# Performance work log

Hardware: AMD Instinct MI355X
Metric: run time of the kernel (lower is better)

## Reference

```python
import jax, jax.numpy as jnp
import numpy as np

C = 128
B = 64
EPS = 1e-6


def _ln2d(x, w, b):
    # LayerNorm over channel dim (NAFNet-style LayerNorm2d), eps=1e-6
    mu = x.mean(axis=1, keepdims=True)
    var = ((x - mu) ** 2).mean(axis=1, keepdims=True)
    return (x - mu) / jnp.sqrt(var + EPS) * w[None, :, None, None] + b[None, :, None, None]


def _conv4(x, w, b):
    # Conv2d kernel 4, stride 4, no padding; NCHW / OIHW
    y = jax.lax.conv_general_dilated(x, w, (4, 4), 'VALID',
                                     dimension_numbers=('NCHW', 'OIHW', 'NCHW'))
    return y + b[None, :, None, None]


def _pixel_shuffle4(x):
    # (B, c*16, H, W) -> (B, c, 4H, 4W), torch PixelShuffle semantics
    b, c16, h, w = x.shape
    c = c16 // 16
    x = x.reshape(b, c, 4, 4, h, w)
    x = x.transpose(0, 1, 4, 2, 5, 3)
    return x.reshape(b, c, h * 4, w * 4)


def setup_inputs() -> dict:
    key = jax.random.key(0)
    ks = jax.random.split(key, 16)
    s = 0.02
    return {
        'x_l': jax.random.normal(ks[0], (B, C, 32, 32), jnp.float32),
        'x_r': jax.random.normal(ks[1], (B, C, 32, 32), jnp.float32),
        'ln_w_l': jnp.ones((C,), jnp.float32), 'ln_b_l': jnp.zeros((C,), jnp.float32),
        'ln_w_r': jnp.ones((C,), jnp.float32), 'ln_b_r': jnp.zeros((C,), jnp.float32),
        'Wl1': jax.random.normal(ks[2], (C, C, 4, 4), jnp.float32) * s,
        'bl1': jnp.zeros((C,), jnp.float32),
        'Wr1': jax.random.normal(ks[3], (C, C, 4, 4), jnp.float32) * s,
        'br1': jnp.zeros((C,), jnp.float32),
        'Wl2': jax.random.normal(ks[4], (C, C, 4, 4), jnp.float32) * s,
        'bl2': jnp.zeros((C,), jnp.float32),
        'Wr2': jax.random.normal(ks[5], (C, C, 4, 4), jnp.float32) * s,
        'br2': jnp.zeros((C,), jnp.float32),
        'pos': jax.random.normal(ks[6], (1, C, 8, 8), jnp.float32),
        'beta': jax.random.normal(ks[7], (1, C, 1, 1), jnp.float32) * s,
        'gamma': jax.random.normal(ks[8], (1, C, 1, 1), jnp.float32) * s,
        'Wl3': jax.random.normal(ks[9], (16 * C, C), jnp.float32) * s,
        'bl3': jnp.zeros((16 * C,), jnp.float32),
        'Wr3': jax.random.normal(ks[10], (16 * C, C), jnp.float32) * s,
        'br3': jnp.zeros((16 * C,), jnp.float32),
    }


def reference(x_l, x_r, ln_w_l, ln_b_l, ln_w_r, ln_b_r, Wl1, bl1, Wr1, br1,
              Wl2, bl2, Wr2, br2, pos, beta, gamma, Wl3, bl3, Wr3, br3):
    c = x_l.shape[1]
    scale = c ** (-0.5)
    B1 = x_l.shape[0]
    B2 = x_r.shape[0]

    Ql = _conv4(_ln2d(x_l, ln_w_l, ln_b_l), Wl1, bl1) + pos  # (B1,c,8,8)
    Qr = _conv4(_ln2d(x_r, ln_w_r, ln_b_r), Wr1, br1) + pos  # (B2,c,8,8)
    h1, w1 = Ql.shape[-2], Ql.shape[-1]
    h2, w2 = Qr.shape[-2], Qr.shape[-1]
    m1, m2 = h1 * w1, h2 * w2

    Qlm = Ql.transpose(0, 2, 3, 1).reshape(B1, m1, c)          # b (h w) c
    Qrm = Qr.transpose(1, 0, 2, 3).reshape(c, B2 * m2)         # c (b h w)
    Vl = (_conv4(x_l, Wl2, bl2) + pos).transpose(0, 2, 3, 1).reshape(B1 * m1, c)
    Vr = (_conv4(x_r, Wr2, br2) + pos).transpose(0, 2, 3, 1).reshape(B2 * m2, c)

    attn = jnp.matmul(Qlm, Qrm) * scale                        # (B1, m1, B2*m2)

    F_r2l = jnp.matmul(jax.nn.softmax(attn * (B2 ** (-0.5)), axis=-1), Vr)
    F_r2l = F_r2l.reshape(B1, h1, w1, c)

    attn2 = attn.reshape(B1, m1, B2, m2).transpose(2, 3, 0, 1).reshape(B2, m2, B1 * m1)
    F_l2r = jnp.matmul(jax.nn.softmax(attn2 * (B1 ** (-0.5)), axis=-1), Vl)
    F_l2r = F_l2r.reshape(B2, h2, w2, c)

    F_r2l = _pixel_shuffle4((jnp.matmul(F_r2l, Wl3.T) + bl3).transpose(0, 3, 1, 2)) * beta
    F_l2r = _pixel_shuffle4((jnp.matmul(F_l2r, Wr3.T) + br3).transpose(0, 3, 1, 2)) * gamma
    return (x_l + F_r2l, x_r + F_l2r)
```

## Files before the change

### kernel.cpp

```cpp
#include <hip/hip_runtime.h>
#include <stdint.h>

using bf16x8 = __attribute__((ext_vector_type(8))) short;
using f32x4  = __attribute__((ext_vector_type(4))) float;

__device__ __forceinline__ unsigned short f2bf(float f) {
  union { float f; uint32_t u; } v; v.f = f;
  uint32_t r = v.u + 0x7FFFu + ((v.u >> 16) & 1u);
  return (unsigned short)(r >> 16);
}
__device__ __forceinline__ uint32_t pk2(float a, float b) {
  return (uint32_t)f2bf(a) | ((uint32_t)f2bf(b) << 16);
}
__device__ __forceinline__ float bf2f(unsigned short s) {
  union { uint32_t u; float f; } v; v.u = ((uint32_t)s) << 16;
  return v.f;
}
__device__ __forceinline__ f32x4 mfma16(bf16x8 a, bf16x8 b, f32x4 c) {
  return __builtin_amdgcn_mfma_f32_16x16x32_bf16(a, b, c, 0, 0, 0);
}

__global__ __launch_bounds__(256) void k_lnstats(
    const float* __restrict__ xl, const float* __restrict__ xr,
    float* __restrict__ muW, float* __restrict__ rsW)
{
  const int bx = blockIdx.x;
  const int side = bx >> 7, rem = bx & 127;
  const int b = rem >> 1, half = rem & 1;
  const float* x = (side ? xr : xl) + (size_t)b * 131072 + half * 512;
  const int t = threadIdx.x;
  const int px = t * 2;
  float s0=0, s1=0, q0=0, q1=0;
#pragma unroll 4
  for (int c = 0; c < 128; ++c) {
    const float2 v = *(const float2*)(x + c*1024 + px);
    s0 += v.x; q0 += v.x*v.x;
    s1 += v.y; q1 += v.y*v.y;
  }
  const int o = (side*64 + b)*1024 + half*512 + px;
  float2 mu, rs;
  mu.x = s0*(1.0f/128.0f); mu.y = s1*(1.0f/128.0f);
  rs.x = rsqrtf(fmaxf(q0*(1.0f/128.0f) - mu.x*mu.x, 0.0f) + 1e-6f);
  rs.y = rsqrtf(fmaxf(q1*(1.0f/128.0f) - mu.y*mu.y, 0.0f) + 1e-6f);
  *(float2*)(muW + o) = mu;
  *(float2*)(rsW + o) = rs;
}

__global__ __launch_bounds__(256) void k_wprep(
    const float* __restrict__ lnwl, const float* __restrict__ lnbl,
    const float* __restrict__ lnwr, const float* __restrict__ lnbr,
    const float* __restrict__ Wl1, const float* __restrict__ bl1,
    const float* __restrict__ Wr1, const float* __restrict__ br1,
    const float* __restrict__ Wl2, const float* __restrict__ Wr2,
    unsigned short* __restrict__ Wq, unsigned short* __restrict__ Wv,
    float* __restrict__ bqW)
{
  const int bx = blockIdx.x;
  const int side = bx >> 7, co = bx & 127;
  const float* W1  = side ? Wr1 : Wl1;
  const float* W2  = side ? Wr2 : Wl2;
  const float* b1  = side ? br1 : bl1;
  const float* lnw = side ? lnwr : lnwl;
  const float* lnb = side ? lnbr : lnbl;
  const int t = threadIdx.x;
  const int ci = t >> 1;
  const float lw = lnw[ci], lb = lnb[ci];

  const size_t dsto = (size_t)(side*32 + (t>>3))*8192 + (size_t)co*64 + (t&7)*8;

  const float* src1 = W1 + (size_t)co*2048 + t*8;
  const float4 a0 = *(const float4*)(src1);
  const float4 a1 = *(const float4*)(src1 + 4);
  float part = (a0.x+a0.y+a0.z+a0.w + a1.x+a1.y+a1.z+a1.w) * lb;
  uint4 pkq;
  pkq.x = pk2(a0.x*lw, a0.y*lw); pkq.y = pk2(a0.z*lw, a0.w*lw);
  pkq.z = pk2(a1.x*lw, a1.y*lw); pkq.w = pk2(a1.z*lw, a1.w*lw);
  *(uint4*)(Wq + dsto) = pkq;

  const float* src2 = W2 + (size_t)co*2048 + t*8;
  const float4 c0 = *(const float4*)(src2);
  const float4 c1 = *(const float4*)(src2 + 4);
  uint4 pkv;
  pkv.x = pk2(c0.x, c0.y); pkv.y = pk2(c0.z, c0.w);
  pkv.z = pk2(c1.x, c1.y); pkv.w = pk2(c1.z, c1.w);
  *(uint4*)(Wv + dsto) = pkv;

  __shared__ float red[4];
  float v = part;
  v += __shfl_down(v, 32, 64); v += __shfl_down(v, 16, 64);
  v += __shfl_down(v, 8, 64);  v += __shfl_down(v, 4, 64);
  v += __shfl_down(v, 2, 64);  v += __shfl_down(v, 1, 64);
  if ((t & 63) == 0) red[t >> 6] = v;
  __syncthreads();
  if (t == 0) bqW[side*128 + co] = b1[co] + red[0] + red[1] + red[2] + red[3];
}

__global__ __launch_bounds__(256) void k_conv(
    const float* __restrict__ xl, const float* __restrict__ xr,
    const unsigned short* __restrict__ Wq, const unsigned short* __restrict__ Wv,
    const float* __restrict__ muW, const float* __restrict__ rsW,
    unsigned short* __restrict__ Cpart)
{
  const int bid = blockIdx.x;
  const int ks = bid & 3;
  const int img = (bid >> 2) & 63;
  const int ctype = bid >> 8;
  const int side = ctype & 1;
  const bool isQ = ctype < 2;
  const float* x = (side ? xr : xl) + (size_t)img * 131072;
  const unsigned short* Bsrc = (isQ ? Wq : Wv) + (size_t)side * 262144;

  const int t = threadIdx.x;
  const int w = t >> 6, l = t & 63, lo = l & 15, g = l >> 4;

  __shared__ __align__(16) unsigned char lds[24576];
  unsigned char* A = lds;
  unsigned char* B = lds + 8192;

  const int cl   = t >> 6;
  const int px0  = (t & 63) * 16;
  const int y    = px0 >> 5;
  const int wr   = y & 3;
  const int pbase = (y >> 2)*8 + ((px0 & 31) >> 2);

  float4 mu4[4], rs4[4];
  if (isQ) {
    const int o = (side*64 + img)*1024 + px0;
#pragma unroll
    for (int i = 0; i < 4; ++i) {
      mu4[i] = *(const float4*)(muW + o + 4*i);
      rs4[i] = *(const float4*)(rsW + o + 4*i);
    }
  }

  const int cout = t >> 1, part = t & 1;
  const int keyB = ((cout ^ (cout >> 3)) & 7) << 4;

  f32x4 acc[4][2];
#pragma unroll
  for (int a = 0; a < 4; ++a) { acc[a][0] = (f32x4)0.0f; acc[a][1] = (f32x4)0.0f; }

  for (int it = 0; it < 8; ++it) {
    const int kb = ks*8 + it;
    __syncthreads();
    {
      const float* xs = x + (size_t)(kb*4 + cl)*1024 + px0;
#pragma unroll
      for (int i = 0; i < 4; ++i) {
        float4 v = *(const float4*)(xs + 4*i);
        if (isQ) {
          v.x = (v.x - mu4[i].x)*rs4[i].x; v.y = (v.y - mu4[i].y)*rs4[i].y;
          v.z = (v.z - mu4[i].z)*rs4[i].z; v.w = (v.w - mu4[i].w)*rs4[i].w;
        }
        const int p = pbase + i;
        int dst = p*128 + cl*32 + wr*8;
        dst ^= ((p ^ (p >> 3)) & 7) << 4;
        *(uint2*)(A + dst) = make_uint2(pk2(v.x, v.y), pk2(v.z, v.w));
      }
    }
    {
      const unsigned short* bs = Bsrc + (size_t)kb*8192 + t*32;
#pragma unroll
      for (int i = 0; i < 4; ++i) {
        const bf16x8 v = *(const bf16x8*)(bs + i*8);
        *(bf16x8*)(B + cout*128 + ((part*64 + i*16) ^ keyB)) = v;
      }
    }
    __syncthreads();
    bf16x8 af[4][2], bfr[2][2];
#pragma unroll
    for (int mf = 0; mf < 4; ++mf) {
      const int row = mf*16 + lo;
      const int key = ((row ^ (row >> 3)) & 7) << 4;
#pragma unroll
      for (int kc = 0; kc < 2; ++kc)
        af[mf][kc] = *(const bf16x8*)(A + row*128 + ((kc*64 + g*16) ^ key));
    }
#pragma unroll
    for (int nf = 0; nf < 2; ++nf) {
      const int row = w*32 + nf*16 + lo;
      const int key = ((row ^ (row >> 3)) & 7) << 4;
#pragma unroll
      for (int kc = 0; kc < 2; ++kc)
        bfr[nf][kc] = *(const bf16x8*)(B + row*128 + ((kc*64 + g*16) ^ key));
    }
    __builtin_amdgcn_s_setprio(1);
#pragma unroll
    for (int kc = 0; kc < 2; ++kc)
#pragma unroll
      for (int nf = 0; nf < 2; ++nf)
#pragma unroll
        for (int mf = 0; mf < 4; ++mf)
          acc[mf][nf] = mfma16(af[mf][kc], bfr[nf][kc], acc[mf][nf]);
    __builtin_amdgcn_s_setprio(0);
  }

  unsigned short* Cp = Cpart + (size_t)bid * 8192;
#pragma unroll
  for (int mf = 0; mf < 4; ++mf)
#pragma unroll
    for (int nf = 0; nf < 2; ++nf) {
      const int c = w*32 + nf*16 + lo;
      const int p0 = mf*16 + g*4;
      *(uint2*)(Cp + c*64 + p0) =
          make_uint2(pk2(acc[mf][nf][0], acc[mf][nf][1]),
                     pk2(acc[mf][nf][2], acc[mf][nf][3]));
    }
}

__global__ __launch_bounds__(256) void k_convred(
    const unsigned short* __restrict__ Cpart,
    const float* __restrict__ bqW,
    const float* __restrict__ bl2, const float* __restrict__ br2,
    const float* __restrict__ pos,
    unsigned short* __restrict__ Qbf, unsigned short* __restrict__ Vtbf)
{
  const int bid2 = blockIdx.x;
  const int ctype = bid2 >> 6, img = bid2 & 63;
  const int side = ctype & 1;
  const bool isQ = ctype < 2;
  const int t = threadIdx.x;

  __shared__ float S[64][130];

  const int c = t >> 1, p0 = (t & 1) * 32;
  {
    float acc[32];
#pragma unroll
    for (int j = 0; j < 32; ++j) acc[j] = 0.f;
#pragma unroll
    for (int s = 0; s < 4; ++s) {
      const unsigned short* Cp = Cpart + ((size_t)(bid2*4 + s))*8192 + c*64 + p0;
#pragma unroll
      for (int j8 = 0; j8 < 4; ++j8) {
        const bf16x8 v = *(const bf16x8*)(Cp + j8*8);
#pragma unroll
        for (int e = 0; e < 8; ++e)
          acc[j8*8 + e] += bf2f((unsigned short)v[e]);
      }
    }
#pragma unroll
    for (int j = 0; j < 32; ++j) S[p0 + j][c] = acc[j];
  }
  __syncthreads();

  if (isQ) {
    const float* bq = bqW + side*128;
    const int p = t >> 2, c0 = (t & 3) * 32;
    const int rot = (t & 3) * 4;
    uint32_t pk[16];
#pragma unroll
    for (int j2 = 0; j2 < 16; ++j2) {
      const int jj = (j2 + rot) & 15;
      const int ca = c0 + jj*2;
      const float2 sv = *(const float2*)(&S[p][ca]);
      const float va = (sv.x + bq[ca]     + pos[ca*64 + p])     * 0.105112052f;
      const float vb = (sv.y + bq[ca + 1] + pos[(ca+1)*64 + p]) * 0.105112052f;
      pk[jj] = pk2(va, vb);
    }
    unsigned short* Qo = Qbf + (size_t)side*524288 + ((size_t)(img*64 + p))*128 + c0;
    *(uint4*)(Qo)      = make_uint4(pk[0],  pk[1],  pk[2],  pk[3]);
    *(uint4*)(Qo + 8)  = make_uint4(pk[4],  pk[5],  pk[6],  pk[7]);
    *(uint4*)(Qo + 16) = make_uint4(pk[8],  pk[9],  pk[10], pk[11]);
    *(uint4*)(Qo + 24) = make_uint4(pk[12], pk[13], pk[14], pk[15]);
  } else {
    const float* b2 = side ? br2 : bl2;
    const float bb = b2[c];
    uint32_t pk[16];
#pragma unroll
    for (int j2 = 0; j2 < 16; ++j2) {
      const int pa = p0 + j2*2;
      const float va = S[pa][c]     + bb + pos[c*64 + pa];
      const float vb = S[pa + 1][c] + bb + pos[c*64 + pa + 1];
      pk[j2] = pk2(va, vb);
    }
    unsigned short* Vo = Vtbf + (size_t)side*524288 + (size_t)c*4096 + img*64 + p0;
    *(uint4*)(Vo)      = make_uint4(pk[0],  pk[1],  pk[2],  pk[3]);
    *(uint4*)(Vo + 8)  = make_uint4(pk[4],  pk[5],  pk[6],  pk[7]);
    *(uint4*)(Vo + 16) = make_uint4(pk[8],  pk[9],  pk[10], pk[11]);
    *(uint4*)(Vo + 24) = make_uint4(pk[12], pk[13], pk[14], pk[15]);
  }
}

__global__ __launch_bounds__(256, 2) void k_attn(
    const unsigned short* __restrict__ Qbf,
    const unsigned short* __restrict__ Vtbf,
    float* __restrict__ Opart,
    float* __restrict__ Lpart)
{
  const int qb = blockIdx.x, ks = blockIdx.y, dir = blockIdx.z;
  const unsigned short* Qp = Qbf  + (size_t)dir*524288;
  const unsigned short* Kp = Qbf  + (size_t)(1-dir)*524288;
  const unsigned short* Vp = Vtbf + (size_t)(1-dir)*524288;

  const int t = threadIdx.x;
  const int w = t >> 6, l = t & 63, lo = l & 15, g = l >> 4;

  __shared__ __align__(16) unsigned char lds[73728];
  unsigned char* ldsP = lds + 65536;
  __shared__ float lred[4][64];

  bf16x8 aq[4][4];
#pragma unroll
  for (int mf = 0; mf < 4; ++mf)
#pragma unroll
    for (int kc = 0; kc < 4; ++kc)
      aq[mf][kc] = *(const bf16x8*)(Qp + (size_t)(qb*64 + mf*16 + lo)*128 + kc*32 + g*8);

  f32x4 o[4][2];
#pragma unroll
  for (int a = 0; a < 4; ++a) { o[a][0] = (f32x4)0.0f; o[a][1] = (f32x4)0.0f; }
  float ls[4][4] = {{0,0,0,0},{0,0,0,0},{0,0,0,0},{0,0,0,0}};

  const int kt0 = ks * 16;

  const int ksrcBase = t ^ ((t >> 4) & 7);
  const int vc    = t >> 3;
  const int vi16  = (t & 7) * 16;
  const int vsoff = (vi16 ^ (((t >> 3) & 7) << 4)) >> 1;

  {
    const uint4* src = (const uint4*)(Kp + (size_t)kt0*8192);
#pragma unroll
    for (int j = 0; j < 4; ++j)
      *(uint4*)(lds + (t + 256*j)*16) = src[ksrcBase + 256*j];
#pragma unroll
    for (int j = 0; j < 4; ++j) {
      const int c = vc + 32*j;
      *(uint4*)(lds + 32768 + c*128 + vi16) =
          *(const uint4*)(Vp + (size_t)c*4096 + kt0*64 + vsoff);
    }
  }
  __syncthreads();

  for (int it = 0; it < 16; ++it) {
    const int cur = it & 1;
    unsigned char* curK = lds + cur*16384;
    unsigned char* curV = lds + 32768 + cur*16384;

    uint4 kr0, kr1, kr2, kr3, vr0, vr1, vr2, vr3;
    if (it < 15) {
      const int kt = kt0 + it + 1;
      const uint4* src = (const uint4*)(Kp + (size_t)kt*8192);
      kr0 = src[ksrcBase];
      kr1 = src[ksrcBase + 256];
      kr2 = src[ksrcBase + 512];
      kr3 = src[ksrcBase + 768];
      const unsigned short* vsrc = Vp + (size_t)kt*64 + vsoff;
      vr0 = *(const uint4*)(vsrc + (size_t)(vc     )*4096);
      vr1 = *(const uint4*)(vsrc + (size_t)(vc + 32)*4096);
      vr2 = *(const uint4*)(vsrc + (size_t)(vc + 64)*4096);
      vr3 = *(const uint4*)(vsrc + (size_t)(vc + 96)*4096);
    }

    f32x4 s[4];
    s[0] = (f32x4)0.0f; s[1] = (f32x4)0.0f; s[2] = (f32x4)0.0f; s[3] = (f32x4)0.0f;
    const int krow = w*16 + lo;
    const int keyk = (krow & 7) << 4;
    __builtin_amdgcn_s_setprio(1);
#pragma unroll
    for (int kc = 0; kc < 4; ++kc) {
      const bf16x8 bk = *(const bf16x8*)(curK + krow*256 + ((kc*64 + g*16) ^ keyk));
#pragma unroll
      for (int mf = 0; mf < 4; ++mf)
        s[mf] = mfma16(aq[mf][kc], bk, s[mf]);
    }
    __builtin_amdgcn_s_setprio(0);

#pragma unroll
    for (int mf = 0; mf < 4; ++mf)
#pragma unroll
      for (int rr = 0; rr < 4; ++rr) {
        const float e = __expf(s[mf][rr]);
        ls[mf][rr] += e;
        const int q = mf*16 + g*4 + rr;
        const int inrow = (w*32 + lo*2) ^ ((q & 7) << 4);
        *(unsigned short*)(ldsP + q*128 + inrow) = f2bf(e);
      }
    __syncthreads();

    __builtin_amdgcn_s_setprio(1);
#pragma unroll
    for (int kd = 0; kd < 2; ++kd) {
      bf16x8 pa[4];
#pragma unroll
      for (int mf = 0; mf < 4; ++mf) {
        const int q = mf*16 + lo;
        pa[mf] = *(const bf16x8*)(ldsP + q*128 + ((kd*64 + g*16) ^ ((q & 7) << 4)));
      }
#pragma unroll
      for (int nf = 0; nf < 2; ++nf) {
        const int c = w*32 + nf*16 + lo;
        const bf16x8 bv = *(const bf16x8*)(curV + c*128 + ((kd*64 + g*16) ^ ((c & 7) << 4)));
#pragma unroll
        for (int mf = 0; mf < 4; ++mf)
          o[mf][nf] = mfma16(pa[mf], bv, o[mf][nf]);
      }
    }
    __builtin_amdgcn_s_setprio(0);

    if (it < 15) {
      unsigned char* nK = lds + (cur ^ 1)*16384;
      unsigned char* nV = lds + 32768 + (cur ^ 1)*16384;
      *(uint4*)(nK + (t      )*16) = kr0;
      *(uint4*)(nK + (t + 256)*16) = kr1;
      *(uint4*)(nK + (t + 512)*16) = kr2;
      *(uint4*)(nK + (t + 768)*16) = kr3;
      *(uint4*)(nV + (vc     )*128 + vi16) = vr0;
      *(uint4*)(nV + (vc + 32)*128 + vi16) = vr1;
      *(uint4*)(nV + (vc + 64)*128 + vi16) = vr2;
      *(uint4*)(nV + (vc + 96)*128 + vi16) = vr3;
    }
    __syncthreads();
  }

#pragma unroll
  for (int mf = 0; mf < 4; ++mf)
#pragma unroll
    for (int rr = 0; rr < 4; ++rr) {
      float v = ls[mf][rr];
      v += __shfl_xor(v, 1, 64);
      v += __shfl_xor(v, 2, 64);
      v += __shfl_xor(v, 4, 64);
      v += __shfl_xor(v, 8, 64);
      ls[mf][rr] = v;
    }
  if (lo == 0) {
#pragma unroll
    for (int mf = 0; mf < 4; ++mf)
#pragma unroll
      for (int rr = 0; rr < 4; ++rr)
        lred[w][mf*16 + g*4 + rr] = ls[mf][rr];
  }
  __syncthreads();

  float* Ob = Opart + (((size_t)dir*64 + qb)*4 + ks)*64*128;
#pragma unroll
  for (int mf = 0; mf < 4; ++mf)
#pragma unroll
    for (int nf = 0; nf < 2; ++nf) {
      const int c = w*32 + nf*16 + lo;
#pragma unroll
      for (int rr = 0; rr < 4; ++rr) {
        const int q = mf*16 + g*4 + rr;
        Ob[q*128 + c] = o[mf][nf][rr];
      }
    }
  if (t < 64)
    Lpart[(((size_t)dir*64 + qb)*4 + ks)*64 + t] =
        lred[0][t] + lred[1][t] + lred[2][t] + lred[3][t];
}

__global__ __launch_bounds__(256) void k_reduce(
    const float* __restrict__ Opart, const float* __restrict__ Lpart,
    unsigned short* __restrict__ Fbf)
{
  const int bid = blockIdx.x;
  const int dir = bid >> 7, rb = bid & 127;
  const int t = threadIdx.x;
  const int qr = t >> 3;
  const int cs = (t & 7) * 16;
  const int r  = rb*32 + qr;
  const int qb = r >> 6, q = r & 63;
  const size_t pb = ((size_t)dir*64 + qb)*4;
  float acc[16];
#pragma unroll
  for (int i = 0; i < 16; ++i) acc[i] = 0.f;
  float lsum = 0.f;
#pragma unroll
  for (int s = 0; s < 4; ++s) {
    const float* Ob = Opart + ((pb + s)*64 + q)*128 + cs;
#pragma unroll
    for (int i = 0; i < 16; i += 4) {
      const float4 v = *(const float4*)(Ob + i);
      acc[i] += v.x; acc[i+1] += v.y; acc[i+2] += v.z; acc[i+3] += v.w;
    }
    lsum += Lpart[(pb + s)*64 + q];
  }
  const float inv = 1.0f / lsum;
  uint32_t pkw[8];
#pragma unroll
  for (int i = 0; i < 8; ++i) pkw[i] = pk2(acc[2*i]*inv, acc[2*i+1]*inv);
  unsigned short* Fo = Fbf + (size_t)dir*524288 + (size_t)r*128 + cs;
  *(uint4*)(Fo)     = make_uint4(pkw[0], pkw[1], pkw[2], pkw[3]);
  *(uint4*)(Fo + 8) = make_uint4(pkw[4], pkw[5], pkw[6], pkw[7]);
}

__global__ __launch_bounds__(256) void k_proj(
    const unsigned short* __restrict__ Fbf,
    const float* __restrict__ Wl3, const float* __restrict__ bl3,
    const float* __restrict__ Wr3, const float* __restrict__ br3,
    const float* __restrict__ beta, const float* __restrict__ gamma,
    const float* __restrict__ xl, const float* __restrict__ xr,
    float* __restrict__ out)
{
  const int nb = blockIdx.x, mb = blockIdx.y, side = blockIdx.z;
  const unsigned short* F = Fbf + (size_t)side*524288;
  const float* W3  = side ? Wr3 : Wl3;
  const float* b3  = side ? br3 : bl3;
  const float* scl = side ? gamma : beta;
  const float* xin = side ? xr : xl;
  float* op = out + (size_t)side*8388608;

  const int t = threadIdx.x;
  const int w = t >> 6, l = t & 63, lo = l & 15, g = l >> 4;

  __shared__ __align__(16) unsigned char Ft[16384];
  __shared__ __align__(16) unsigned char B3[32768];

  {
    const uint4* src = (const uint4*)(F + (size_t)mb*8192);
#pragma unroll
    for (int j = 0; j < 4; ++j) {
      const int idx = t + 256*j;
      const int dst = idx*16;
      const int row = dst >> 8;
      *(uint4*)(Ft + dst) = src[(dst ^ ((row & 7) << 4)) >> 4];
    }
  }
  {
    const int nl = t >> 1, half = t & 1;
    const float* wsrc = W3 + (size_t)(nb*128 + nl)*128 + half*64;
#pragma unroll
    for (int ch = 0; ch < 8; ++ch) {
      const float4 v0 = *(const float4*)(wsrc + ch*8);
      const float4 v1 = *(const float4*)(wsrc + ch*8 + 4);
      uint4 pk;
      pk.x = pk2(v0.x,v0.y); pk.y = pk2(v0.z,v0.w);
      pk.z = pk2(v1.x,v1.y); pk.w = pk2(v1.z,v1.w);
      const int inrow = (half*128 + ch*16) ^ ((nl & 7) << 4);
      *(uint4*)(B3 + nl*256 + inrow) = pk;
    }
  }
  __syncthreads();

  f32x4 acc[4][2];
#pragma unroll
  for (int a=0;a<4;a++) { acc[a][0] = (f32x4)0.0f; acc[a][1] = (f32x4)0.0f; }

  bf16x8 af[4][4];
#pragma unroll
  for (int mf = 0; mf < 4; ++mf) {
    const int row = mf*16 + lo;
#pragma unroll
    for (int kc = 0; kc < 4; ++kc)
      af[mf][kc] = *(const bf16x8*)(Ft + row*256 + ((kc*64 + g*16) ^ ((row & 7) << 4)));
  }
#pragma unroll
  for (int kc = 0; kc < 4; ++kc)
#pragma unroll
    for (int nf = 0; nf < 2; ++nf) {
      const int n = w*32 + nf*16 + lo;
      const bf16x8 bb = *(const bf16x8*)(B3 + n*256 + ((kc*64 + g*16) ^ ((n & 7) << 4)));
#pragma unroll
      for (int mf = 0; mf < 4; ++mf)
        acc[mf][nf] = mfma16(af[mf][kc], bb, acc[mf][nf]);
    }

#pragma unroll
  for (int mf = 0; mf < 4; ++mf)
#pragma unroll
    for (int nf = 0; nf < 2; ++nf) {
      const int n16 = nb*128 + w*32 + nf*16 + lo;
      const int c = n16 >> 4, r4 = (n16 >> 2) & 3, sc = n16 & 3;
      const float scc = scl[c];
      const float bb3 = b3[n16];
#pragma unroll
      for (int rr = 0; rr < 4; ++rr) {
        const int pi = mf*16 + g*4 + rr;
        const int h = pi >> 3, wc = pi & 7;
        const size_t oidx = ((size_t)(mb*128 + c))*1024 + (size_t)(h*4 + r4)*32 + wc*4 + sc;
        op[oidx] = xin[oidx] + scc*(acc[mf][nf][rr] + bb3);
      }
    }
}

extern "C" void kernel_launch(void* const* d_in, const int* in_sizes, int n_in,
                              void* d_out, int out_size, void* d_ws, size_t ws_size,
                              hipStream_t stream) {
  (void)in_sizes; (void)n_in; (void)out_size; (void)ws_size;
  const float* xl   = (const float*)d_in[0];
  const float* xr   = (const float*)d_in[1];
  const float* lnwl = (const float*)d_in[2];
  const float* lnbl = (const float*)d_in[3];
  const float* lnwr = (const float*)d_in[4];
  const float* lnbr = (const float*)d_in[5];
  const float* Wl1  = (const float*)d_in[6];
  const float* bl1  = (const float*)d_in[7];
  const float* Wr1  = (const float*)d_in[8];
  const float* br1  = (const float*)d_in[9];
  const float* Wl2  = (const float*)d_in[10];
  const float* bl2  = (const float*)d_in[11];
  const float* Wr2  = (const float*)d_in[12];
  const float* br2  = (const float*)d_in[13];
  const float* pos  = (const float*)d_in[14];
  const float* beta = (const float*)d_in[15];
  const float* gamma= (const float*)d_in[16];
  const float* Wl3  = (const float*)d_in[17];
  const float* bl3  = (const float*)d_in[18];
  const float* Wr3  = (const float*)d_in[19];
  const float* br3  = (const float*)d_in[20];

  float* muW = (float*)d_ws;
  float* rsW = muW + 131072;
  float* bqW = rsW + 131072;
  unsigned short* Wq   = (unsigned short*)(bqW + 256);
  unsigned short* Wv   = Wq + 524288;
  unsigned short* Qbf  = Wv + 524288;
  unsigned short* Vtbf = Qbf + 1048576;
  unsigned short* Fbf  = Vtbf + 1048576;
  unsigned short* Cpart = Fbf + 1048576;
  float* Opart = (float*)Cpart;
  float* Lpart = (float*)(Cpart + 8388608);

  k_lnstats<<<256, 256, 0, stream>>>(xl, xr, muW, rsW);
  k_wprep<<<256, 256, 0, stream>>>(lnwl, lnbl, lnwr, lnbr,
      Wl1, bl1, Wr1, br1, Wl2, Wr2, Wq, Wv, bqW);
  k_conv<<<1024, 256, 0, stream>>>(xl, xr, Wq, Wv, muW, rsW, Cpart);
  k_convred<<<256, 256, 0, stream>>>(Cpart, bqW, bl2, br2, pos, Qbf, Vtbf);
  k_attn<<<dim3(64, 4, 2), 256, 0, stream>>>(Qbf, Vtbf, Opart, Lpart);
  k_reduce<<<256, 256, 0, stream>>>(Opart, Lpart, Fbf);
  k_proj<<<dim3(16, 64, 2), 256, 0, stream>>>(Fbf, Wl3, bl3, Wr3, br3,
      beta, gamma, xl, xr, (float*)d_out);
}
```

Baseline: 135.8 us.

## Pre-convert W3 to bf16 once and stage proj epilogue through LDS for coalesced stores

Adds a k_w3prep kernel that converts Wl3/Wr3 to bf16 once, so each of the 2048 k_proj blocks loads half the weight bytes and skips repeated fp32-to-bf16 packing. The k_proj epilogue now writes scaled results into a padded LDS buffer and then performs float4 coalesced residual reads and output writes, replacing the scattered scalar pixel-shuffle stores. This costs an extra launch, extra workspace, larger shared memory per block (48KB) and an additional barrier.

```diff
diff --git a/kernel.cpp b/kernel.cpp
--- a/kernel.cpp
+++ b/kernel.cpp
@@ -93,6 +93,17 @@
   if ((t & 63) == 0) red[t >> 6] = v;
   __syncthreads();
   if (t == 0) bqW[side*128 + co] = b1[co] + red[0] + red[1] + red[2] + red[3];
+}
+
+__global__ __launch_bounds__(256) void k_w3prep(
+    const float* __restrict__ Wl3, const float* __restrict__ Wr3,
+    unsigned short* __restrict__ W3bf)
+{
+  const int b = blockIdx.x;
+  const float* src = (b < 256 ? Wl3 : Wr3) + (size_t)(b & 255) * 1024;
+  const int t = threadIdx.x;
+  const float4 v = *(const float4*)(src + t*4);
+  *(uint2*)(W3bf + (size_t)b*1024 + t*4) = make_uint2(pk2(v.x, v.y), pk2(v.z, v.w));
 }
 
 __global__ __launch_bounds__(256) void k_conv(
@@ -488,28 +499,30 @@
 
 __global__ __launch_bounds__(256) void k_proj(
     const unsigned short* __restrict__ Fbf,
-    const float* __restrict__ Wl3, const float* __restrict__ bl3,
-    const float* __restrict__ Wr3, const float* __restrict__ br3,
+    const unsigned short* __restrict__ W3bf,
+    const float* __restrict__ bl3, const float* __restrict__ br3,
     const float* __restrict__ beta, const float* __restrict__ gamma,
     const float* __restrict__ xl, const float* __restrict__ xr,
     float* __restrict__ out)
 {
   const int nb = blockIdx.x, mb = blockIdx.y, side = blockIdx.z;
-  const unsigned short* F = Fbf + (size_t)side*524288;
-  const float* W3  = side ? Wr3 : Wl3;
-  const float* b3  = side ? br3 : bl3;
+  const unsigned short* F  = Fbf + (size_t)side*524288 + (size_t)mb*8192;
+  const unsigned short* W3 = W3bf + (size_t)side*262144 + (size_t)nb*16384;
+  const float* b3  = (side ? br3 : bl3) + nb*128;
   const float* scl = side ? gamma : beta;
-  const float* xin = side ? xr : xl;
-  float* op = out + (size_t)side*8388608;
+  const float* xin = (side ? xr : xl) + (size_t)mb*131072;
+  float* op = out + (size_t)side*8388608 + (size_t)mb*131072;
 
   const int t = threadIdx.x;
   const int w = t >> 6, l = t & 63, lo = l & 15, g = l >> 4;
 
-  __shared__ __align__(16) unsigned char Ft[16384];
-  __shared__ __align__(16) unsigned char B3[32768];
+  __shared__ __align__(16) unsigned char lds[49152];
+  unsigned char* Ft = lds;
+  unsigned char* B3 = lds + 16384;
+  float* Sf = (float*)lds;
 
   {
-    const uint4* src = (const uint4*)(F + (size_t)mb*8192);
+    const uint4* src = (const uint4*)F;
 #pragma unroll
     for (int j = 0; j < 4; ++j) {
       const int idx = t + 256*j;
@@ -520,16 +533,12 @@
   }
   {
     const int nl = t >> 1, half = t & 1;
-    const float* wsrc = W3 + (size_t)(nb*128 + nl)*128 + half*64;
+    const unsigned short* wsrc = W3 + (size_t)nl*128 + half*64;
 #pragma unroll
     for (int ch = 0; ch < 8; ++ch) {
-      const float4 v0 = *(const float4*)(wsrc + ch*8);
-      const float4 v1 = *(const float4*)(wsrc + ch*8 + 4);
-      uint4 pk;
-      pk.x = pk2(v0.x,v0.y); pk.y = pk2(v0.z,v0.w);
-      pk.z = pk2(v1.x,v1.y); pk.w = pk2(v1.z,v1.w);
+      const uint4 v = *(const uint4*)(wsrc + ch*8);
       const int inrow = (half*128 + ch*16) ^ ((nl & 7) << 4);
-      *(uint4*)(B3 + nl*256 + inrow) = pk;
+      *(uint4*)(B3 + nl*256 + inrow) = v;
     }
   }
   __syncthreads();
@@ -557,22 +566,38 @@
         acc[mf][nf] = mfma16(af[mf][kc], bb, acc[mf][nf]);
     }
 
-#pragma unroll
-  for (int mf = 0; mf < 4; ++mf)
+  __syncthreads();
+
+  {
+    const int r4 = (lo >> 2) & 3, sc = lo & 3;
 #pragma unroll
     for (int nf = 0; nf < 2; ++nf) {
-      const int n16 = nb*128 + w*32 + nf*16 + lo;
-      const int c = n16 >> 4, r4 = (n16 >> 2) & 3, sc = n16 & 3;
-      const float scc = scl[c];
+      const int cl = w*2 + nf;
+      const int n16 = w*32 + nf*16 + lo;
+      const float scc = scl[nb*8 + cl];
       const float bb3 = b3[n16];
 #pragma unroll
-      for (int rr = 0; rr < 4; ++rr) {
-        const int pi = mf*16 + g*4 + rr;
-        const int h = pi >> 3, wc = pi & 7;
-        const size_t oidx = ((size_t)(mb*128 + c))*1024 + (size_t)(h*4 + r4)*32 + wc*4 + sc;
-        op[oidx] = xin[oidx] + scc*(acc[mf][nf][rr] + bb3);
-      }
-    }
+      for (int mf = 0; mf < 4; ++mf)
+#pragma unroll
+        for (int rr = 0; rr < 4; ++rr) {
+          const int pi = mf*16 + g*4 + rr;
+          const int h = pi >> 3, wc = pi & 7;
+          Sf[cl*1032 + h*128 + r4*32 + wc*4 + sc] = scc*(acc[mf][nf][rr] + bb3);
+        }
+    }
+  }
+  __syncthreads();
+
+#pragma unroll
+  for (int j = 0; j < 8; ++j) {
+    const int pix = t*4;
+    const float4 s = *(const float4*)(Sf + j*1032 + pix);
+    const size_t gaddr = (size_t)(nb*8 + j)*1024 + pix;
+    const float4 xv = *(const float4*)(xin + gaddr);
+    float4 r;
+    r.x = xv.x + s.x; r.y = xv.y + s.y; r.z = xv.z + s.z; r.w = xv.w + s.w;
+    *(float4*)(op + gaddr) = r;
+  }
 }
 
 extern "C" void kernel_launch(void* const* d_in, const int* in_sizes, int n_in,
@@ -609,17 +634,19 @@
   unsigned short* Qbf  = Wv + 524288;
   unsigned short* Vtbf = Qbf + 1048576;
   unsigned short* Fbf  = Vtbf + 1048576;
-  unsigned short* Cpart = Fbf + 1048576;
+  unsigned short* W3bf = Fbf + 1048576;
+  unsigned short* Cpart = W3bf + 524288;
   float* Opart = (float*)Cpart;
   float* Lpart = (float*)(Cpart + 8388608);
 
   k_lnstats<<<256, 256, 0, stream>>>(xl, xr, muW, rsW);
   k_wprep<<<256, 256, 0, stream>>>(lnwl, lnbl, lnwr, lnbr,
       Wl1, bl1, Wr1, br1, Wl2, Wr2, Wq, Wv, bqW);
+  k_w3prep<<<512, 256, 0, stream>>>(Wl3, Wr3, W3bf);
   k_conv<<<1024, 256, 0, stream>>>(xl, xr, Wq, Wv, muW, rsW, Cpart);
   k_convred<<<256, 256, 0, stream>>>(Cpart, bqW, bl2, br2, pos, Qbf, Vtbf);
   k_attn<<<dim3(64, 4, 2), 256, 0, stream>>>(Qbf, Vtbf, Opart, Lpart);
   k_reduce<<<256, 256, 0, stream>>>(Opart, Lpart, Fbf);
-  k_proj<<<dim3(16, 64, 2), 256, 0, stream>>>(Fbf, Wl3, bl3, Wr3, br3,
+  k_proj<<<dim3(16, 64, 2), 256, 0, stream>>>(Fbf, W3bf, bl3, br3,
       beta, gamma, xl, xr, (float*)d_out);
 }
```

New measurement: 121.6 us. 10.4% less time.
